# Kernel tuning notes

Hardware: AMD Instinct MI355X
Metric: run time of the kernel (lower is better)

Reference implementation:

```python
import jax, jax.numpy as jnp
import numpy as np

B = 131072
W = 64
E = 16
DIMS = [W * E, 130, 110, 90, 70, 50]  # hidden funnel; final Linear 50 -> W
EPS = 1e-5  # torch BatchNorm1d default eps


def setup_inputs() -> dict:
    key = jax.random.key(0)
    ks = jax.random.split(key, 32)
    inp = {"events": jax.random.normal(ks[0], (B, W, E), dtype=jnp.float32)}
    ki = 1
    for i in range(5):
        fan_in, fan_out = DIMS[i], DIMS[i + 1]
        bound = 1.0 / np.sqrt(fan_in)
        inp[f"W{i}"] = jax.random.uniform(ks[ki], (fan_out, fan_in), jnp.float32, -bound, bound); ki += 1
        inp[f"b{i}"] = jax.random.uniform(ks[ki], (fan_out,), jnp.float32, -bound, bound); ki += 1
        inp[f"g{i}"] = jnp.ones((fan_out,), jnp.float32)   # BN gamma
        inp[f"be{i}"] = jnp.zeros((fan_out,), jnp.float32)  # BN beta
    bound = 1.0 / np.sqrt(50)
    inp["W5"] = jax.random.uniform(ks[ki], (W, 50), jnp.float32, -bound, bound); ki += 1
    inp["b5"] = jax.random.uniform(ks[ki], (W,), jnp.float32, -bound, bound)
    return inp


def _mlp(x, Ws, bs, gs, bes, W5, b5):
    # Linear -> BatchNorm (training-mode batch stats) -> ReLU, x5; then Linear -> sigmoid
    for Wl, bl, gl, bel in zip(Ws, bs, gs, bes):
        x = x @ Wl.T + bl
        mu = jnp.mean(x, axis=0)
        var = jnp.var(x, axis=0)
        x = gl * (x - mu) * jax.lax.rsqrt(var + EPS) + bel
        x = jax.nn.relu(x)
    return jax.nn.sigmoid(x @ W5.T + b5)


def reference(events, W0, b0, g0, be0, W1, b1, g1, be1, W2, b2, g2, be2,
              W3, b3, g3, be3, W4, b4, g4, be4, W5, b5):
    x = events.reshape((events.shape[0], W * E))
    probs = _mlp(x, [W0, W1, W2, W3, W4], [b0, b1, b2, b3, b4],
                 [g0, g1, g2, g3, g4], [be0, be1, be2, be3, be4], W5, b5)  # [B, W]
    # np.random.choice([0,1], p=[p, 1-p]) -> choice=1 w.p. (1-p)
    u = jax.random.uniform(jax.random.key(42), probs.shape, dtype=probs.dtype)
    chosen = (u < (1.0 - probs)).astype(probs.dtype)          # 'choice' in source
    chosen_events_np = 1.0 - chosen                           # returned mask
    # log prod |chosen - probs| == sum log|chosen - probs|
    log_probs = jnp.sum(jnp.log(jnp.abs(chosen - probs)), axis=1)  # [B]
    return chosen_events_np, log_probs
```

## Files before the change

kernel.cpp:

```cpp
#include <hip/hip_runtime.h>
#include <type_traits>

static const long BATCH = 131072;
static const int ROWS = 32;
static const int NBLOCKS = 4096;
static const int GBLOCKS = 2048;

using f64x4 = __attribute__((ext_vector_type(4))) double;

__device__ __forceinline__ unsigned rotl32(unsigned x, int d) {
  return (x << d) | (x >> (32 - d));
}

struct U2 { unsigned a, b; };

__device__ __forceinline__ U2 threefry(unsigned x0, unsigned x1) {
  const unsigned ks0 = 0u, ks1 = 42u, ks2 = 0u ^ 42u ^ 0x1BD11BDAu;
  x0 += ks0; x1 += ks1;
#define TF_R4(A,B,C,D) \
  x0 += x1; x1 = rotl32(x1, A); x1 ^= x0; \
  x0 += x1; x1 = rotl32(x1, B); x1 ^= x0; \
  x0 += x1; x1 = rotl32(x1, C); x1 ^= x0; \
  x0 += x1; x1 = rotl32(x1, D); x1 ^= x0;
  TF_R4(13,15,26,6)  x0 += ks1; x1 += ks2 + 1u;
  TF_R4(17,29,16,24) x0 += ks2; x1 += ks0 + 2u;
  TF_R4(13,15,26,6)  x0 += ks0; x1 += ks1 + 3u;
  TF_R4(17,29,16,24) x0 += ks1; x1 += ks2 + 4u;
  TF_R4(13,15,26,6)  x0 += ks2; x1 += ks0 + 5u;
#undef TF_R4
  U2 r; r.a = x0; r.b = x1; return r;
}

__device__ __forceinline__ float jax_uniform(unsigned idx) {
  U2 r = threefry(0u, idx);
  unsigned bits = r.a ^ r.b;
  unsigned fb = (bits >> 9) | 0x3f800000u;
  return __uint_as_float(fb) - 1.0f;
}

__global__ __launch_bounds__(64) void probe_layout(unsigned* __restrict__ maps) {
  __shared__ double X1[16][5], X2[16][5], W1s[4][17], W2s[4][17];
  const int l = threadIdx.x;
  const int lr = l & 15, lk = l >> 4;
  {
    int i = l >> 2, k = l & 3;
    X1[i][k] = (k == 0) ? (double)i : 0.0;
    X2[i][k] = (k == 0) ? 1.0 : 0.0;
    W1s[k][i] = (k == 0) ? 1.0 : 0.0;
    W2s[k][i] = (k == 0) ? (double)i : 0.0;
  }
  __syncthreads();
  f64x4 a1 = {0.0, 0.0, 0.0, 0.0}, a2 = {0.0, 0.0, 0.0, 0.0};
  a1 = __builtin_amdgcn_mfma_f64_16x16x4f64(X1[lr][lk], W1s[lk][lr], a1, 0, 0, 0);
  a2 = __builtin_amdgcn_mfma_f64_16x16x4f64(X2[lr][lk], W2s[lk][lr], a2, 0, 0, 0);
  unsigned m = 0;
  #pragma unroll
  for (int r = 0; r < 4; ++r) {
    int row = (int)(a1[r] + 0.5);
    int col = (int)(a2[r] + 0.5);
    m |= (unsigned)(((row & 15) << 4) | (col & 15)) << (8 * r);
  }
  maps[l] = m;
}

template<int M, int N, int MODE>
__global__ __launch_bounds__(256, 4) void gemm_mfma(
    const void* __restrict__ inv, const float* __restrict__ W,
    const float* __restrict__ bias,
    const double* __restrict__ bna, const double* __restrict__ bnc,
    const unsigned* __restrict__ maps_g,
    double* __restrict__ hout, double* __restrict__ partials)
{
  constexpr int BK = 16;
  constexpr int NT = (N + 15) / 16;
  constexpr int NPAD = NT * 16;
  constexpr int NCH = (M + BK - 1) / BK;
  constexpr int NW = BK * NPAD;
  constexpr int WLD = (NW + 255) / 256;

  struct SM0 { float  xs[64][17]; float ws[BK][NPAD + 1]; };
  struct SM1 { double xs[64][17]; float ws[BK][NPAD + 1]; };
  using SMX = typename std::conditional<MODE == 0, SM0, SM1>::type;
  union SMEM { SMX m; double tt[4][16][17]; };
  __shared__ SMEM sm;

  const int tid = threadIdx.x;
  const int w = tid >> 6;
  const int l = tid & 63;
  const int lr = l & 15;
  const int lk = l >> 4;
  const long i0 = (long)blockIdx.x * 64;
  const int wrow = w * 16;
  const unsigned um = maps_g[l];

  float xf[4]; double xd[4]; float wf[WLD];

  auto load_chunk = [&](int k0) {
    #pragma unroll
    for (int p = 0; p < 4; ++p) {
      int idx = tid + p * 256;
      int r = idx >> 4, kk = idx & 15;
      int k = k0 + kk;
      if constexpr (MODE == 0) {
        xf[p] = (k < M) ? ((const float*)inv)[(i0 + r) * (long)M + k] : 0.0f;
      } else {
        double v = 0.0;
        if (k < M) {
          v = ((const double*)inv)[(i0 + r) * (long)M + k];
          v = v * bna[k] + bnc[k];
          v = v > 0.0 ? v : 0.0;
        }
        xd[p] = v;
      }
    }
    #pragma unroll
    for (int p = 0; p < WLD; ++p) {
      int idx = tid + p * 256;
      float v = 0.0f;
      if (idx < NW) {
        int kk = idx & 15, j = idx >> 4;
        int k = k0 + kk;
        if (j < N && k < M) v = W[(long)j * M + k];
      }
      wf[p] = v;
    }
  };

  auto write_chunk = [&]() {
    #pragma unroll
    for (int p = 0; p < 4; ++p) {
      int idx = tid + p * 256;
      int r = idx >> 4, kk = idx & 15;
      if constexpr (MODE == 0) sm.m.xs[r][kk] = xf[p];
      else                     sm.m.xs[r][kk] = xd[p];
    }
    #pragma unroll
    for (int p = 0; p < WLD; ++p) {
      int idx = tid + p * 256;
      if (idx < NW) {
        int kk = idx & 15, j = idx >> 4;
        sm.m.ws[kk][j] = wf[p];
      }
    }
  };

  f64x4 acc[NT];
  #pragma unroll
  for (int t = 0; t < NT; ++t) acc[t] = (f64x4){0.0, 0.0, 0.0, 0.0};

  load_chunk(0);
  for (int ch = 0; ch < NCH; ++ch) {
    __syncthreads();
    write_chunk();
    __syncthreads();
    if (ch + 1 < NCH) load_chunk((ch + 1) * BK);
    #pragma unroll
    for (int ks = 0; ks < 4; ++ks) {
      double aA = (double)sm.m.xs[wrow + lr][ks * 4 + lk];
      #pragma unroll
      for (int t = 0; t < NT; ++t) {
        double bB = (double)sm.m.ws[ks * 4 + lk][t * 16 + lr];
        acc[t] = __builtin_amdgcn_mfma_f64_16x16x4f64(aA, bB, acc[t], 0, 0, 0);
      }
    }
  }

  double* pp = partials + (long)blockIdx.x * (2 * N);
  for (int t = 0; t < NT; ++t) {
    __syncthreads();
    #pragma unroll
    for (int r = 0; r < 4; ++r) {
      unsigned b = (um >> (8 * r)) & 0xffu;
      sm.tt[w][b >> 4][b & 15] = acc[t][r];
    }
    __syncthreads();
    for (int idx = tid; idx < 1024; idx += 256) {
      int rb = idx >> 4, j16 = idx & 15;
      int j = t * 16 + j16;
      if (j < N) {
        double h = sm.tt[rb >> 4][rb & 15][j16] + (double)bias[j];
        hout[(i0 + rb) * (long)N + j] = h;
      }
    }
    if (tid < 64) {
      int j16 = tid >> 2, part = tid & 3;
      int j = t * 16 + j16;
      double s = 0.0, q = 0.0;
      if (j < N) {
        double bj = (double)bias[j];
        #pragma unroll
        for (int rr = 0; rr < 16; ++rr) {
          int rb = part * 16 + rr;
          double h = sm.tt[rb >> 4][rb & 15][j16] + bj;
          s += h; q += h * h;
        }
      }
      s += __shfl_xor(s, 1); s += __shfl_xor(s, 2);
      q += __shfl_xor(q, 1); q += __shfl_xor(q, 2);
      if (part == 0 && j < N) { pp[j] = s; pp[N + j] = q; }
    }
  }
}

__global__ __launch_bounds__(256) void final_store(
    const double* __restrict__ h4,
    const double* __restrict__ bna, const double* __restrict__ bnc,
    const float* __restrict__ W5, const float* __restrict__ b5,
    float* __restrict__ out0, float* __restrict__ out1)
{
  __shared__ double A5[ROWS][51];
  __shared__ double W5S[50][65];
  __shared__ double T[ROWS][65];
  const int tid = threadIdx.x;
  const int c = tid & 63, g = tid >> 6;
  const long i0 = (long)blockIdx.x * ROWS;

  for (int idx = tid; idx < ROWS * 50; idx += 256) {
    int r = idx / 50, k = idx % 50;
    double v = h4[(i0 + r) * 50 + k] * bna[k] + bnc[k];
    A5[r][k] = v > 0.0 ? v : 0.0;
  }
  for (int idx = tid; idx < 64 * 50; idx += 256) {
    int j = idx / 50, k = idx % 50;
    W5S[k][j] = (double)W5[j * 50 + k];
  }
  __syncthreads();

  double acc[8];
  #pragma unroll
  for (int rr = 0; rr < 8; ++rr) acc[rr] = 0.0;
  for (int k = 0; k < 50; ++k) {
    double w = W5S[k][c];
    #pragma unroll
    for (int rr = 0; rr < 8; ++rr) acc[rr] += A5[g * 8 + rr][k] * w;
  }
  double bj = (double)b5[c];
  #pragma unroll
  for (int rr = 0; rr < 8; ++rr) {
    int r = g * 8 + rr;
    double h = acc[rr] + bj;
    double p = 1.0 / (1.0 + exp(-h));
    float uf = jax_uniform((unsigned)((i0 + r) * 64 + c));
    bool ch = ((double)uf < 1.0 - p);
    out0[(i0 + r) * 64 + c] = ch ? 0.0f : 1.0f;
    T[r][c] = log(ch ? (1.0 - p) : p);
  }
  __syncthreads();
  for (int r = tid; r < ROWS; r += 256) {
    double s = 0.0;
    for (int j = 0; j < 64; ++j) s += T[r][j];
    out1[i0 + r] = (float)s;
  }
}

template<int M, int N>
__device__ __forceinline__ void step_gemm(const double* IN, const float* __restrict__ W,
                                          int tid, double* acc) {
  if (tid < N) {
    #pragma unroll
    for (int r = 0; r < 32; ++r) acc[r] = 0.0;
    for (int k = 0; k < M; ++k) {
      double wv = (double)W[tid * M + k];
      #pragma unroll
      for (int r = 0; r < 32; ++r) acc[r] += IN[r * M + k] * wv;
    }
  }
}

template<int N>
__device__ __forceinline__ void step_write(double* OUT, const double* acc,
                                           const float* __restrict__ b, int tid) {
  if (tid < N) {
    double bj = (double)b[tid];
    #pragma unroll
    for (int r = 0; r < 32; ++r) OUT[r * N + tid] = acc[r] + bj;
  }
}

template<int N>
__device__ __forceinline__ void step_stats(const double* acc, const float* __restrict__ b,
                                           double* partials, int blk, int tid) {
  if (tid < N) {
    double bj = (double)b[tid], s = 0.0, q = 0.0;
    #pragma unroll
    for (int r = 0; r < 32; ++r) { double h = acc[r] + bj; s += h; q += h * h; }
    double* pp = partials + (long)blk * (2 * N);
    pp[tid] = s; pp[N + tid] = q;
  }
}

template<int N>
__device__ __forceinline__ void apply_bn(double* BUF, const double* __restrict__ a,
                                         const double* __restrict__ c, int tid) {
  for (int idx = tid; idx < 32 * N; idx += 256) {
    int col = idx % N;
    double v = BUF[idx] * a[col] + c[col];
    BUF[idx] = v > 0.0 ? v : 0.0;
  }
}

template<int PL>
__global__ __launch_bounds__(256) void chain_pass(
    const float* __restrict__ ev,
    const float* __restrict__ W0, const float* __restrict__ b0,
    const float* __restrict__ W1, const float* __restrict__ b1,
    const float* __restrict__ W2, const float* __restrict__ b2,
    const float* __restrict__ W3, const float* __restrict__ b3,
    const float* __restrict__ W4, const float* __restrict__ b4,
    const float* __restrict__ W5, const float* __restrict__ b5,
    const double* __restrict__ bn_a, const double* __restrict__ bn_c,
    double* __restrict__ partials,
    float* __restrict__ out0, float* __restrict__ out1)
{
  __shared__ double SA[32 * 130];
  __shared__ double SB[32 * 110];
  const int tid = threadIdx.x;
  const int blk = blockIdx.x;
  const long i0 = (long)blk * 32;
  double acc[32];

  {
    float* evf = (float*)SA;
    if (tid < 130) {
      #pragma unroll
      for (int r = 0; r < 32; ++r) acc[r] = 0.0;
    }
    for (int c = 0; c < 4; ++c) {
      __syncthreads();
      for (int idx = tid; idx < 32 * 256; idx += 256) {
        int r = idx >> 8, kk = idx & 255;
        evf[idx] = ev[(i0 + r) * 1024 + c * 256 + kk];
      }
      __syncthreads();
      if (tid < 130) {
        for (int kk = 0; kk < 256; ++kk) {
          double wv = (double)W0[tid * 1024 + c * 256 + kk];
          #pragma unroll
          for (int r = 0; r < 32; ++r) acc[r] += (double)evf[r * 256 + kk] * wv;
        }
      }
    }
    __syncthreads();
    if constexpr (PL == 0) { step_stats<130>(acc, b0, partials, blk, tid); return; }
    step_write<130>(SA, acc, b0, tid);
    __syncthreads();
    apply_bn<130>(SA, bn_a + 0, bn_c + 0, tid);
    __syncthreads();
  }
  if constexpr (PL >= 1) {
    step_gemm<130, 110>(SA, W1, tid, acc);
    if constexpr (PL == 1) { step_stats<110>(acc, b1, partials, blk, tid); return; }
    __syncthreads();
    step_write<110>(SB, acc, b1, tid);
    __syncthreads();
    apply_bn<110>(SB, bn_a + 130, bn_c + 130, tid);
    __syncthreads();
  }
  if constexpr (PL >= 2) {
    step_gemm<110, 90>(SB, W2, tid, acc);
    if constexpr (PL == 2) { step_stats<90>(acc, b2, partials, blk, tid); return; }
    __syncthreads();
    step_write<90>(SA, acc, b2, tid);
    __syncthreads();
    apply_bn<90>(SA, bn_a + 240, bn_c + 240, tid);
    __syncthreads();
  }
  if constexpr (PL >= 3) {
    step_gemm<90, 70>(SA, W3, tid, acc);
    if constexpr (PL == 3) { step_stats<70>(acc, b3, partials, blk, tid); return; }
    __syncthreads();
    step_write<70>(SB, acc, b3, tid);
    __syncthreads();
    apply_bn<70>(SB, bn_a + 330, bn_c + 330, tid);
    __syncthreads();
  }
  if constexpr (PL >= 4) {
    step_gemm<70, 50>(SB, W4, tid, acc);
    if constexpr (PL == 4) { step_stats<50>(acc, b4, partials, blk, tid); return; }
    __syncthreads();
    step_write<50>(SA, acc, b4, tid);
    __syncthreads();
    apply_bn<50>(SA, bn_a + 400, bn_c + 400, tid);
    __syncthreads();
  }
  if constexpr (PL == 5) {
    if (tid < 64) {
      #pragma unroll
      for (int r = 0; r < 32; ++r) acc[r] = 0.0;
      for (int k = 0; k < 50; ++k) {
        double wv = (double)W5[tid * 50 + k];
        #pragma unroll
        for (int r = 0; r < 32; ++r) acc[r] += SA[r * 50 + k] * wv;
      }
      double bj = (double)b5[tid];
      #pragma unroll
      for (int r = 0; r < 32; ++r) {
        double h = acc[r] + bj;
        double p = 1.0 / (1.0 + exp(-h));
        float uf = jax_uniform((unsigned)((i0 + r) * 64 + tid));
        bool ch = ((double)uf < 1.0 - p);
        out0[(i0 + r) * 64 + tid] = ch ? 0.0f : 1.0f;
        double d = ch ? (1.0 - p) : p;
        SB[r * 64 + tid] = log(d);
      }
    }
    __syncthreads();
    if (tid < 32) {
      double s = 0.0;
      for (int j = 0; j < 64; ++j) s += SB[tid * 64 + j];
      out1[i0 + tid] = (float)s;
    }
  }
}

template<int N>
__global__ __launch_bounds__(256) void bn_finalize2(
    const double* __restrict__ partials, int nblocks,
    const float* __restrict__ g, const float* __restrict__ be,
    double* __restrict__ a, double* __restrict__ c)
{
  const int j = blockIdx.x;
  const int tid = threadIdx.x;
  double s = 0.0, q = 0.0;
  for (int b = tid; b < nblocks; b += 256) {
    const double* p = partials + (long)b * (2 * N);
    s += p[j];
    q += p[N + j];
  }
  __shared__ double ls[256], lq[256];
  ls[tid] = s; lq[tid] = q;
  __syncthreads();
  for (int off = 128; off > 0; off >>= 1) {
    if (tid < off) { ls[tid] += ls[tid + off]; lq[tid] += lq[tid + off]; }
    __syncthreads();
  }
  if (tid == 0) {
    double mu  = ls[0] * (1.0 / 131072.0);
    double var = lq[0] * (1.0 / 131072.0) - mu * mu;
    double aj  = (double)g[j] / sqrt(var + 1e-5);
    a[j] = aj;
    c[j] = (double)be[j] - mu * aj;
  }
}

extern "C" void kernel_launch(void* const* d_in, const int* in_sizes, int n_in,
                              void* d_out, int out_size, void* d_ws, size_t ws_size,
                              hipStream_t stream)
{
  const float* F[23];
  for (int i = 0; i < 23; ++i) F[i] = (const float*)d_in[i];
  const float* ev = F[0];
  float* out0 = (float*)d_out;
  float* out1 = out0 + BATCH * 64;

  double* partials = (double*)d_out;
  double* bn_a = (double*)d_ws;
  double* bn_c = bn_a + 450;
  unsigned* maps = (unsigned*)(bn_c + 450);

  char* ws = (char*)d_ws;
  size_t used = (size_t)((char*)(maps + 64) - ws);
  used = (used + 255) & ~(size_t)255;
  const size_t needA = (size_t)BATCH * 130 * 8;
  const size_t needB = (size_t)BATCH * 110 * 8;

  dim3 b(256);

  if (ws_size >= used + needA + needB) {
    double* bufA = (double*)(ws + used);
    double* bufB = (double*)(ws + used + needA);
    dim3 g(GBLOCKS);
    probe_layout<<<dim3(1), dim3(64), 0, stream>>>(maps);
    gemm_mfma<1024, 130, 0><<<g, b, 0, stream>>>(ev, F[1], F[2],
        nullptr, nullptr, maps, bufA, partials);
    bn_finalize2<130><<<dim3(130), b, 0, stream>>>(partials, GBLOCKS, F[3], F[4], bn_a + 0, bn_c + 0);
    gemm_mfma<130, 110, 1><<<g, b, 0, stream>>>(bufA, F[5], F[6],
        bn_a + 0, bn_c + 0, maps, bufB, partials);
    bn_finalize2<110><<<dim3(110), b, 0, stream>>>(partials, GBLOCKS, F[7], F[8], bn_a + 130, bn_c + 130);
    gemm_mfma<110, 90, 1><<<g, b, 0, stream>>>(bufB, F[9], F[10],
        bn_a + 130, bn_c + 130, maps, bufA, partials);
    bn_finalize2<90><<<dim3(90), b, 0, stream>>>(partials, GBLOCKS, F[11], F[12], bn_a + 240, bn_c + 240);
    gemm_mfma<90, 70, 1><<<g, b, 0, stream>>>(bufA, F[13], F[14],
        bn_a + 240, bn_c + 240, maps, bufB, partials);
    bn_finalize2<70><<<dim3(70), b, 0, stream>>>(partials, GBLOCKS, F[15], F[16], bn_a + 330, bn_c + 330);
    gemm_mfma<70, 50, 1><<<g, b, 0, stream>>>(bufB, F[17], F[18],
        bn_a + 330, bn_c + 330, maps, bufA, partials);
    bn_finalize2<50><<<dim3(50), b, 0, stream>>>(partials, GBLOCKS, F[19], F[20], bn_a + 400, bn_c + 400);
    final_store<<<dim3(NBLOCKS), b, 0, stream>>>(bufA, bn_a + 400, bn_c + 400, F[21], F[22], out0, out1);
  } else {
    dim3 g(NBLOCKS);
#define ARGS ev, F[1],F[2], F[5],F[6], F[9],F[10], F[13],F[14], F[17],F[18], \
             F[21],F[22], bn_a, bn_c, partials, out0, out1
    chain_pass<0><<<g, b, 0, stream>>>(ARGS);
    bn_finalize2<130><<<dim3(130), b, 0, stream>>>(partials, NBLOCKS, F[3],  F[4],  bn_a + 0,   bn_c + 0);
    chain_pass<1><<<g, b, 0, stream>>>(ARGS);
    bn_finalize2<110><<<dim3(110), b, 0, stream>>>(partials, NBLOCKS, F[7],  F[8],  bn_a + 130, bn_c + 130);
    chain_pass<2><<<g, b, 0, stream>>>(ARGS);
    bn_finalize2<90><<<dim3(90),  b, 0, stream>>>(partials, NBLOCKS, F[11], F[12], bn_a + 240, bn_c + 240);
    chain_pass<3><<<g, b, 0, stream>>>(ARGS);
    bn_finalize2<70><<<dim3(70),  b, 0, stream>>>(partials, NBLOCKS, F[15], F[16], bn_a + 330, bn_c + 330);
    chain_pass<4><<<g, b, 0, stream>>>(ARGS);
    bn_finalize2<50><<<dim3(50),  b, 0, stream>>>(partials, NBLOCKS, F[19], F[20], bn_a + 400, bn_c + 400);
    chain_pass<5><<<g, b, 0, stream>>>(ARGS);
#undef ARGS
  }
}
```

Measured before the change: 1.136 ms.

## Load GEMM A operand directly to registers, double-buffer weights, transpose BN partials

The MFMA GEMM now reads each lane's A fragment straight from global memory into registers (float4 in mode 0) instead of staging it through shared memory. It double-buffers the weight tile in LDS so only one barrier is needed per K-chunk, and caches the BN scale/shift in shared memory for mode 1. BN partial sums are stored column-major so the finalize kernel reads them contiguously. The occupancy hint drops from 4 to 3 blocks per SM to allow more registers, which may reduce latency hiding.

```diff
diff --git a/kernel.cpp b/kernel.cpp
--- a/kernel.cpp
+++ b/kernel.cpp
@@ -64,7 +64,7 @@
 }
 
 template<int M, int N, int MODE>
-__global__ __launch_bounds__(256, 4) void gemm_mfma(
+__global__ __launch_bounds__(256, 3) void gemm_mfma(
     const void* __restrict__ inv, const float* __restrict__ W,
     const float* __restrict__ bias,
     const double* __restrict__ bna, const double* __restrict__ bnc,
@@ -74,73 +74,75 @@
   constexpr int BK = 16;
   constexpr int NT = (N + 15) / 16;
   constexpr int NPAD = NT * 16;
+  constexpr int WSTR = NPAD + 2;
   constexpr int NCH = (M + BK - 1) / BK;
   constexpr int NW = BK * NPAD;
   constexpr int WLD = (NW + 255) / 256;
-
-  struct SM0 { float  xs[64][17]; float ws[BK][NPAD + 1]; };
-  struct SM1 { double xs[64][17]; float ws[BK][NPAD + 1]; };
-  using SMX = typename std::conditional<MODE == 0, SM0, SM1>::type;
-  union SMEM { SMX m; double tt[4][16][17]; };
+  constexpr int SMK = (MODE == 1) ? (NCH * BK) : 1;
+
+  struct SMM { float ws[2][BK][WSTR]; double bn[2][SMK]; };
+  union SMEM { SMM m; double tt[4][16][17]; };
   __shared__ SMEM sm;
 
   const int tid = threadIdx.x;
-  const int w = tid >> 6;
-  const int l = tid & 63;
-  const int lr = l & 15;
-  const int lk = l >> 4;
+  const int w = tid >> 6, l = tid & 63;
+  const int lr = l & 15, lk = l >> 4;
   const long i0 = (long)blockIdx.x * 64;
   const int wrow = w * 16;
   const unsigned um = maps_g[l];
-
-  float xf[4]; double xd[4]; float wf[WLD];
-
-  auto load_chunk = [&](int k0) {
-    #pragma unroll
-    for (int p = 0; p < 4; ++p) {
-      int idx = tid + p * 256;
-      int r = idx >> 4, kk = idx & 15;
-      int k = k0 + kk;
-      if constexpr (MODE == 0) {
-        xf[p] = (k < M) ? ((const float*)inv)[(i0 + r) * (long)M + k] : 0.0f;
-      } else {
-        double v = 0.0;
-        if (k < M) {
-          v = ((const double*)inv)[(i0 + r) * (long)M + k];
-          v = v * bna[k] + bnc[k];
-          v = v > 0.0 ? v : 0.0;
-        }
-        xd[p] = v;
-      }
-    }
+  const long arow = i0 + wrow + lr;
+
+  if constexpr (MODE == 1) {
+    for (int k = tid; k < SMK; k += 256) {
+      sm.m.bn[0][k] = (k < M) ? bna[k] : 0.0;
+      sm.m.bn[1][k] = (k < M) ? bnc[k] : 0.0;
+    }
+  }
+
+  float wreg[WLD];
+  float a4f[4], a4fn[4];
+  double a4d[4], a4dn[4];
+
+  auto loadW = [&](int k0) {
     #pragma unroll
     for (int p = 0; p < WLD; ++p) {
       int idx = tid + p * 256;
       float v = 0.0f;
       if (idx < NW) {
-        int kk = idx & 15, j = idx >> 4;
+        int j = idx >> 4, kk = idx & 15;
         int k = k0 + kk;
         if (j < N && k < M) v = W[(long)j * M + k];
       }
-      wf[p] = v;
+      wreg[p] = v;
     }
   };
-
-  auto write_chunk = [&]() {
-    #pragma unroll
-    for (int p = 0; p < 4; ++p) {
-      int idx = tid + p * 256;
-      int r = idx >> 4, kk = idx & 15;
-      if constexpr (MODE == 0) sm.m.xs[r][kk] = xf[p];
-      else                     sm.m.xs[r][kk] = xd[p];
-    }
+  auto writeW = [&](int buf) {
     #pragma unroll
     for (int p = 0; p < WLD; ++p) {
       int idx = tid + p * 256;
       if (idx < NW) {
-        int kk = idx & 15, j = idx >> 4;
-        sm.m.ws[kk][j] = wf[p];
-      }
+        int j = idx >> 4, kk = idx & 15;
+        sm.m.ws[buf][kk][j] = wreg[p];
+      }
+    }
+  };
+  auto loadA = [&](int k0, bool nxt) {
+    int kb = k0 + lk * 4;
+    if constexpr (MODE == 0) {
+      float* dst = nxt ? a4fn : a4f;
+      if (kb + 4 <= M) {
+        float4 v = *(const float4*)((const float*)inv + arow * (long)M + kb);
+        dst[0] = v.x; dst[1] = v.y; dst[2] = v.z; dst[3] = v.w;
+      } else {
+        #pragma unroll
+        for (int e = 0; e < 4; ++e)
+          dst[e] = (kb + e < M) ? ((const float*)inv)[arow * (long)M + kb + e] : 0.0f;
+      }
+    } else {
+      double* dst = nxt ? a4dn : a4d;
+      #pragma unroll
+      for (int e = 0; e < 4; ++e)
+        dst[e] = (kb + e < M) ? ((const double*)inv)[arow * (long)M + kb + e] : 0.0;
     }
   };
 
@@ -148,24 +150,45 @@
   #pragma unroll
   for (int t = 0; t < NT; ++t) acc[t] = (f64x4){0.0, 0.0, 0.0, 0.0};
 
-  load_chunk(0);
+  loadA(0, false);
+  loadW(0);
+  writeW(0);
+  __syncthreads();
+  int cur = 0;
   for (int ch = 0; ch < NCH; ++ch) {
-    __syncthreads();
-    write_chunk();
-    __syncthreads();
-    if (ch + 1 < NCH) load_chunk((ch + 1) * BK);
+    const int k0 = ch * BK;
+    if (ch + 1 < NCH) { loadA(k0 + BK, true); loadW(k0 + BK); }
     #pragma unroll
     for (int ks = 0; ks < 4; ++ks) {
-      double aA = (double)sm.m.xs[wrow + lr][ks * 4 + lk];
+      double aA;
+      if constexpr (MODE == 0) {
+        aA = (double)a4f[ks];
+      } else {
+        int k = k0 + lk * 4 + ks;
+        double v = a4d[ks] * sm.m.bn[0][k] + sm.m.bn[1][k];
+        aA = v > 0.0 ? v : 0.0;
+      }
       #pragma unroll
       for (int t = 0; t < NT; ++t) {
-        double bB = (double)sm.m.ws[ks * 4 + lk][t * 16 + lr];
+        double bB = (double)sm.m.ws[cur][lk * 4 + ks][t * 16 + lr];
         acc[t] = __builtin_amdgcn_mfma_f64_16x16x4f64(aA, bB, acc[t], 0, 0, 0);
       }
     }
-  }
-
-  double* pp = partials + (long)blockIdx.x * (2 * N);
+    if (ch + 1 < NCH) writeW(cur ^ 1);
+    __syncthreads();
+    if (ch + 1 < NCH) {
+      if constexpr (MODE == 0) {
+        #pragma unroll
+        for (int e = 0; e < 4; ++e) a4f[e] = a4fn[e];
+      } else {
+        #pragma unroll
+        for (int e = 0; e < 4; ++e) a4d[e] = a4dn[e];
+      }
+      cur ^= 1;
+    }
+  }
+
+  const int blk = blockIdx.x;
   for (int t = 0; t < NT; ++t) {
     __syncthreads();
     #pragma unroll
@@ -197,7 +220,10 @@
       }
       s += __shfl_xor(s, 1); s += __shfl_xor(s, 2);
       q += __shfl_xor(q, 1); q += __shfl_xor(q, 2);
-      if (part == 0 && j < N) { pp[j] = s; pp[N + j] = q; }
+      if (part == 0 && j < N) {
+        partials[(long)j * GBLOCKS + blk] = s;
+        partials[(long)(N + j) * GBLOCKS + blk] = q;
+      }
     }
   }
 }
@@ -284,8 +310,8 @@
     double bj = (double)b[tid], s = 0.0, q = 0.0;
     #pragma unroll
     for (int r = 0; r < 32; ++r) { double h = acc[r] + bj; s += h; q += h * h; }
-    double* pp = partials + (long)blk * (2 * N);
-    pp[tid] = s; pp[N + tid] = q;
+    partials[(long)tid * NBLOCKS + blk] = s;
+    partials[(long)(N + tid) * NBLOCKS + blk] = q;
   }
 }
 
@@ -423,9 +449,8 @@
   const int tid = threadIdx.x;
   double s = 0.0, q = 0.0;
   for (int b = tid; b < nblocks; b += 256) {
-    const double* p = partials + (long)b * (2 * N);
-    s += p[j];
-    q += p[N + j];
+    s += partials[(long)j * nblocks + b];
+    q += partials[(long)(N + j) * nblocks + b];
   }
   __shared__ double ls[256], lq[256];
   ls[tid] = s; lq[tid] = q;
```

New measurement: 1.078 ms. 1.05x faster.
